# Optimization experiments

Measured on AMD Instinct MI355X. Metric: run time of the kernel, lower is better.

Reference implementation:

```python
import jax, jax.numpy as jnp
import numpy as np

N, M, D_M, D_S = 200000, 100000, 128, 128


def setup_inputs() -> dict:
    key = jax.random.key(0)
    ks = jax.random.split(key, 7)
    messages = jax.random.normal(ks[0], (M, D_M), dtype=jnp.float32)
    S = jax.random.normal(ks[1], (N, D_S), dtype=jnp.float32)
    # torch GRUCell default init: U(-1/sqrt(d_s), 1/sqrt(d_s))
    bound = 1.0 / np.sqrt(D_S)
    W_ih = jax.random.uniform(ks[2], (3 * D_S, D_M), minval=-bound, maxval=bound, dtype=jnp.float32)
    W_hh = jax.random.uniform(ks[3], (3 * D_S, D_S), minval=-bound, maxval=bound, dtype=jnp.float32)
    b_ih = jax.random.uniform(ks[4], (3 * D_S,), minval=-bound, maxval=bound, dtype=jnp.float32)
    b_hh = jax.random.uniform(ks[5], (3 * D_S,), minval=-bound, maxval=bound, dtype=jnp.float32)
    # dict keys are unique -> draw M unique node indices
    idx = jax.random.permutation(ks[6], N)[:M].astype(jnp.int64)
    return {"messages": messages, "S": S, "W_ih": W_ih, "W_hh": W_hh,
            "b_ih": b_ih, "b_hh": b_hh, "idx": idx}


def gru_cell(x, h, W_ih, W_hh, b_ih, b_hh):
    # torch.nn.GRUCell math, gate order (r, z, n)
    gi = x @ W_ih.T + b_ih          # [M, 3*d_s]
    gh = h @ W_hh.T + b_hh          # [M, 3*d_s]
    gi_r, gi_z, gi_n = jnp.split(gi, 3, axis=-1)
    gh_r, gh_z, gh_n = jnp.split(gh, 3, axis=-1)
    r = jax.nn.sigmoid(gi_r + gh_r)
    z = jax.nn.sigmoid(gi_z + gh_z)
    n = jnp.tanh(gi_n + r * gh_n)
    return (1.0 - z) * n + z * h


def reference(messages, S, W_ih, W_hh, b_ih, b_hh, idx):
    h = S[idx]                                     # gather [M, d_s]
    h_new = gru_cell(messages, h, W_ih, W_hh, b_ih, b_hh)
    # original initializes S_next = ones_like(S), then scatters updates
    return jnp.ones_like(S).at[idx].set(h_new)
```

## Files before the change

kernel.cpp:

```cpp
#include <hip/hip_runtime.h>
#include <hip/hip_bf16.h>
#include <stdint.h>

#define MM 100000
#define NN 200000
#define DD 128
#define BM 32
#define NT 3125
#define GRID 512

typedef __attribute__((ext_vector_type(8))) short short8;
typedef __attribute__((ext_vector_type(4))) float f32x4;
typedef __attribute__((ext_vector_type(2))) unsigned int u32x2;

__device__ __forceinline__ unsigned short f2bf(float f) {
    union { float f; uint32_t u; } v; v.f = f;
    return (unsigned short)((v.u + 0x7FFFu + ((v.u >> 16) & 1u)) >> 16);
}
__device__ __forceinline__ unsigned int pack_bf2(float lo, float hi) {
    union { float f; uint32_t u; } a, b; a.f = lo; b.f = hi;
    return ((a.u + 0x8000u) >> 16) | ((b.u + 0x8000u) & 0xFFFF0000u);
}
__device__ __forceinline__ float bf2f(unsigned short s) {
    union { uint32_t u; float f; } v; v.u = ((uint32_t)s) << 16;
    return v.f;
}
__device__ __forceinline__ float sigmoidf(float x) {
    return 1.0f / (1.0f + __expf(-x));
}
__device__ __forceinline__ float tanh_fast(float x) {
    return 2.0f / (1.0f + __expf(-2.0f * x)) - 1.0f;
}

__global__ void fill_ones(f32x4* __restrict__ out, int n4) {
    int i = blockIdx.x * blockDim.x + threadIdx.x;
    int stride = gridDim.x * blockDim.x;
    f32x4 ones = {1.f, 1.f, 1.f, 1.f};
    for (; i < n4; i += stride) out[i] = ones;
}

__global__ void clear_mark(uint32_t* __restrict__ mark32) {
    int i = blockIdx.x * blockDim.x + threadIdx.x;
    if (i < (NN + 3) / 4) mark32[i] = 0;
}

__global__ void mark_rows(const int* __restrict__ idx, uint8_t* __restrict__ mark) {
    int m = blockIdx.x * blockDim.x + threadIdx.x;
    if (m < MM) mark[idx[m]] = 1;
}

__global__ void conv_w(const float* __restrict__ wih, const float* __restrict__ whh,
                       unsigned short* __restrict__ dst) {
    int i = blockIdx.x * blockDim.x + threadIdx.x;
    if (i < 3 * DD * DD) {
        dst[i] = f2bf(wih[i]);
        dst[3 * DD * DD + i] = f2bf(whh[i]);
    }
}

template <bool WBF16>
__device__ __forceinline__ short8 load_wfrag(const void* W, int row, int kbase) {
    if constexpr (WBF16) {
        const unsigned short* p = (const unsigned short*)W;
        return *reinterpret_cast<const short8*>(p + (size_t)row * DD + kbase);
    } else {
        const float* p = (const float*)W + (size_t)row * DD + kbase;
        f32x4 a = *reinterpret_cast<const f32x4*>(p);
        f32x4 b = *reinterpret_cast<const f32x4*>(p + 4);
        short8 r;
        r[0] = (short)f2bf(a[0]); r[1] = (short)f2bf(a[1]);
        r[2] = (short)f2bf(a[2]); r[3] = (short)f2bf(a[3]);
        r[4] = (short)f2bf(b[0]); r[5] = (short)f2bf(b[1]);
        r[6] = (short)f2bf(b[2]); r[7] = (short)f2bf(b[3]);
        return r;
    }
}

template <bool WBF16>
__global__ __launch_bounds__(512, 4) void gru_kernel(
    const float* __restrict__ msgs, const float* __restrict__ S,
    const void* __restrict__ Wih, const void* __restrict__ Whh,
    const float* __restrict__ b_ih, const float* __restrict__ b_hh,
    const int* __restrict__ idx, float* __restrict__ out,
    const uint8_t* __restrict__ mark)
{
    __shared__ unsigned short Xl[2][BM][136];
    __shared__ unsigned short Hl[2][BM][136];
    __shared__ int Il[2][BM];

    const int tid = threadIdx.x;
    const int wave = tid >> 6;
    const int lane = tid & 63;
    const int l15 = lane & 15;
    const int lk  = lane >> 4;
    const int c   = wave * 16 + l15;

    const float br   = b_ih[c] + b_hh[c];
    const float bz   = b_ih[DD + c] + b_hh[DD + c];
    const float bn_i = b_ih[2 * DD + c];
    const float bn_h = b_hh[2 * DD + c];

    const int srow = tid >> 5;
    const int sch  = tid & 31;

    int t = blockIdx.x;

    int si_g[2], si_n[2];
    f32x4 px[2], ph[2];
    #pragma unroll
    for (int it = 0; it < 2; ++it) si_g[it] = idx[t * BM + srow + it * 16];
    #pragma unroll
    for (int it = 0; it < 2; ++it) {
        int m = t * BM + srow + it * 16;
        px[it] = *reinterpret_cast<const f32x4*>(msgs + (size_t)m * DD + sch * 4);
        ph[it] = *reinterpret_cast<const f32x4*>(S + (size_t)si_g[it] * DD + sch * 4);
    }
    if (t + GRID < NT) {
        #pragma unroll
        for (int it = 0; it < 2; ++it) si_n[it] = idx[(t + GRID) * BM + srow + it * 16];
    }

    int p = 0;
    for (; t < NT; t += GRID) {
        const bool hasn = (t + GRID) < NT;

        #pragma unroll
        for (int it = 0; it < 2; ++it) {
            u32x2 xw, hw;
            xw[0] = pack_bf2(px[it][0], px[it][1]);
            xw[1] = pack_bf2(px[it][2], px[it][3]);
            hw[0] = pack_bf2(ph[it][0], ph[it][1]);
            hw[1] = pack_bf2(ph[it][2], ph[it][3]);
            *reinterpret_cast<u32x2*>(&Xl[p][srow + it * 16][sch * 4]) = xw;
            *reinterpret_cast<u32x2*>(&Hl[p][srow + it * 16][sch * 4]) = hw;
            if (sch == 0) Il[p][srow + it * 16] = si_g[it];
        }
        __syncthreads();

        if (hasn) {
            #pragma unroll
            for (int it = 0; it < 2; ++it) {
                int m = (t + GRID) * BM + srow + it * 16;
                px[it] = *reinterpret_cast<const f32x4*>(msgs + (size_t)m * DD + sch * 4);
                ph[it] = *reinterpret_cast<const f32x4*>(S + (size_t)si_n[it] * DD + sch * 4);
                si_g[it] = si_n[it];
            }
            if (t + 2 * GRID < NT) {
                #pragma unroll
                for (int it = 0; it < 2; ++it)
                    si_n[it] = idx[(t + 2 * GRID) * BM + srow + it * 16];
            }
        }

        f32x4 accR[2], accZ[2], accNi[2], accNh[2];
        #pragma unroll
        for (int mt = 0; mt < 2; ++mt) {
            accR[mt] = (f32x4){0.f, 0.f, 0.f, 0.f};
            accZ[mt] = (f32x4){0.f, 0.f, 0.f, 0.f};
            accNi[mt] = (f32x4){0.f, 0.f, 0.f, 0.f};
            accNh[mt] = (f32x4){0.f, 0.f, 0.f, 0.f};
        }
        #pragma unroll
        for (int ks = 0; ks < 4; ++ks) {
            const int kb = ks * 32 + lk * 8;
            short8 ax[2], ah[2];
            #pragma unroll
            for (int mt = 0; mt < 2; ++mt) {
                ax[mt] = *reinterpret_cast<const short8*>(&Xl[p][mt * 16 + l15][kb]);
                ah[mt] = *reinterpret_cast<const short8*>(&Hl[p][mt * 16 + l15][kb]);
            }
            short8 bRi = load_wfrag<WBF16>(Wih, c, kb);
            short8 bRh = load_wfrag<WBF16>(Whh, c, kb);
            short8 bZi = load_wfrag<WBF16>(Wih, DD + c, kb);
            short8 bZh = load_wfrag<WBF16>(Whh, DD + c, kb);
            short8 bNi = load_wfrag<WBF16>(Wih, 2 * DD + c, kb);
            short8 bNh = load_wfrag<WBF16>(Whh, 2 * DD + c, kb);
            #pragma unroll
            for (int mt = 0; mt < 2; ++mt) {
                accR[mt]  = __builtin_amdgcn_mfma_f32_16x16x32_bf16(ax[mt], bRi, accR[mt], 0, 0, 0);
                accR[mt]  = __builtin_amdgcn_mfma_f32_16x16x32_bf16(ah[mt], bRh, accR[mt], 0, 0, 0);
                accZ[mt]  = __builtin_amdgcn_mfma_f32_16x16x32_bf16(ax[mt], bZi, accZ[mt], 0, 0, 0);
                accZ[mt]  = __builtin_amdgcn_mfma_f32_16x16x32_bf16(ah[mt], bZh, accZ[mt], 0, 0, 0);
                accNi[mt] = __builtin_amdgcn_mfma_f32_16x16x32_bf16(ax[mt], bNi, accNi[mt], 0, 0, 0);
                accNh[mt] = __builtin_amdgcn_mfma_f32_16x16x32_bf16(ah[mt], bNh, accNh[mt], 0, 0, 0);
            }
        }

        #pragma unroll
        for (int mt = 0; mt < 2; ++mt) {
            #pragma unroll
            for (int j = 0; j < 4; ++j) {
                int mloc = mt * 16 + lk * 4 + j;
                float r = sigmoidf(accR[mt][j] + br);
                float z = sigmoidf(accZ[mt][j] + bz);
                float n = tanh_fast(accNi[mt][j] + bn_i + r * (accNh[mt][j] + bn_h));
                float h = bf2f(Hl[p][mloc][c]);
                uint32_t off = (uint32_t)Il[p][mloc] * (uint32_t)DD + (uint32_t)c;
                out[off] = (1.f - z) * n + z * h;
            }
        }
        p ^= 1;
    }

    if (mark != nullptr) {
        f32x4 ones = {1.f, 1.f, 1.f, 1.f};
        f32x4* out4 = (f32x4*)out;
        int g = blockIdx.x * 512 + tid;
        for (int i = g; i < NN * 32; i += GRID * 512)
            if (!mark[i >> 5]) out4[i] = ones;
    }
}

extern "C" void kernel_launch(void* const* d_in, const int* in_sizes, int n_in,
                              void* d_out, int out_size, void* d_ws, size_t ws_size,
                              hipStream_t stream) {
    const float* msgs  = (const float*)d_in[0];
    const float* S     = (const float*)d_in[1];
    const float* W_ih  = (const float*)d_in[2];
    const float* W_hh  = (const float*)d_in[3];
    const float* b_ih  = (const float*)d_in[4];
    const float* b_hh  = (const float*)d_in[5];
    const int*   idx   = (const int*)d_in[6];
    float* out = (float*)d_out;

    const size_t wbytes = (size_t)2 * 3 * DD * DD * sizeof(unsigned short);
    const size_t need = wbytes + NN + 256;

    if (ws_size >= need) {
        unsigned short* wbf = (unsigned short*)d_ws;
        uint8_t* mark = (uint8_t*)d_ws + wbytes;
        clear_mark<<<(NN / 4 + 511) / 512, 512, 0, stream>>>((uint32_t*)mark);
        mark_rows<<<(MM + 511) / 512, 512, 0, stream>>>(idx, mark);
        conv_w<<<(3 * DD * DD + 255) / 256, 256, 0, stream>>>(W_ih, W_hh, wbf);
        gru_kernel<true><<<GRID, 512, 0, stream>>>(msgs, S, wbf, wbf + 3 * DD * DD,
                                                   b_ih, b_hh, idx, out, mark);
    } else {
        fill_ones<<<2048, 256, 0, stream>>>((f32x4*)out, NN * DD / 4);
        gru_kernel<false><<<GRID, 512, 0, stream>>>(msgs, S, W_ih, W_hh,
                                                    b_ih, b_hh, idx, out, nullptr);
    }
}
```

Before: 295.3 us.

## Replace persistent double-buffered GRU loop with one block per 32-row tile

Drops the persistent grid-stride loop, with its register prefetch and double-buffered LDS, and launches one block per 32-row tile (3125 blocks). Each block loads its tile, runs the MFMAs split into an input-side and a hidden-side phase so fewer weight fragments are live at once, then applies the gate epilogue. The aim is to lower register and LDS pressure and let the hardware scheduler overlap tiles across many resident blocks instead of relying on manual prefetch. The trade-off is that weight fragments are reloaded per block rather than per loop iteration, and the ones-fill tail now strides over a much larger grid.

After: 287.4 us. 1.03x faster.

```diff
diff --git a/kernel.cpp b/kernel.cpp
--- a/kernel.cpp
+++ b/kernel.cpp
@@ -6,8 +6,7 @@
 #define NN 200000
 #define DD 128
 #define BM 32
-#define NT 3125
-#define GRID 512
+#define NB 3125
 
 typedef __attribute__((ext_vector_type(8))) short short8;
 typedef __attribute__((ext_vector_type(4))) float f32x4;
@@ -84,108 +83,84 @@
     const int* __restrict__ idx, float* __restrict__ out,
     const uint8_t* __restrict__ mark)
 {
-    __shared__ unsigned short Xl[2][BM][136];
-    __shared__ unsigned short Hl[2][BM][136];
-    __shared__ int Il[2][BM];
+    __shared__ unsigned short Xl[BM][136];
+    __shared__ unsigned short Hl[BM][136];
+    __shared__ int Il[BM];
 
     const int tid = threadIdx.x;
-    const int wave = tid >> 6;
-    const int lane = tid & 63;
-    const int l15 = lane & 15;
-    const int lk  = lane >> 4;
-    const int c   = wave * 16 + l15;
-
-    const float br   = b_ih[c] + b_hh[c];
-    const float bz   = b_ih[DD + c] + b_hh[DD + c];
-    const float bn_i = b_ih[2 * DD + c];
-    const float bn_h = b_hh[2 * DD + c];
-
-    const int srow = tid >> 5;
-    const int sch  = tid & 31;
-
-    int t = blockIdx.x;
-
-    int si_g[2], si_n[2];
-    f32x4 px[2], ph[2];
-    #pragma unroll
-    for (int it = 0; it < 2; ++it) si_g[it] = idx[t * BM + srow + it * 16];
-    #pragma unroll
-    for (int it = 0; it < 2; ++it) {
-        int m = t * BM + srow + it * 16;
-        px[it] = *reinterpret_cast<const f32x4*>(msgs + (size_t)m * DD + sch * 4);
-        ph[it] = *reinterpret_cast<const f32x4*>(S + (size_t)si_g[it] * DD + sch * 4);
-    }
-    if (t + GRID < NT) {
-        #pragma unroll
-        for (int it = 0; it < 2; ++it) si_n[it] = idx[(t + GRID) * BM + srow + it * 16];
-    }
-
-    int p = 0;
-    for (; t < NT; t += GRID) {
-        const bool hasn = (t + GRID) < NT;
-
+    const int t   = blockIdx.x;
+
+    {
+        const int srow = tid >> 5;
+        const int sch  = tid & 31;
         #pragma unroll
         for (int it = 0; it < 2; ++it) {
+            int m = t * BM + srow + it * 16;
+            int si = idx[m];
+            f32x4 xv = *reinterpret_cast<const f32x4*>(msgs + (size_t)m * DD + sch * 4);
+            f32x4 hv = *reinterpret_cast<const f32x4*>(S + (size_t)si * DD + sch * 4);
             u32x2 xw, hw;
-            xw[0] = pack_bf2(px[it][0], px[it][1]);
-            xw[1] = pack_bf2(px[it][2], px[it][3]);
-            hw[0] = pack_bf2(ph[it][0], ph[it][1]);
-            hw[1] = pack_bf2(ph[it][2], ph[it][3]);
-            *reinterpret_cast<u32x2*>(&Xl[p][srow + it * 16][sch * 4]) = xw;
-            *reinterpret_cast<u32x2*>(&Hl[p][srow + it * 16][sch * 4]) = hw;
-            if (sch == 0) Il[p][srow + it * 16] = si_g[it];
-        }
-        __syncthreads();
-
-        if (hasn) {
-            #pragma unroll
-            for (int it = 0; it < 2; ++it) {
-                int m = (t + GRID) * BM + srow + it * 16;
-                px[it] = *reinterpret_cast<const f32x4*>(msgs + (size_t)m * DD + sch * 4);
-                ph[it] = *reinterpret_cast<const f32x4*>(S + (size_t)si_n[it] * DD + sch * 4);
-                si_g[it] = si_n[it];
-            }
-            if (t + 2 * GRID < NT) {
-                #pragma unroll
-                for (int it = 0; it < 2; ++it)
-                    si_n[it] = idx[(t + 2 * GRID) * BM + srow + it * 16];
-            }
-        }
-
-        f32x4 accR[2], accZ[2], accNi[2], accNh[2];
-        #pragma unroll
-        for (int mt = 0; mt < 2; ++mt) {
-            accR[mt] = (f32x4){0.f, 0.f, 0.f, 0.f};
-            accZ[mt] = (f32x4){0.f, 0.f, 0.f, 0.f};
-            accNi[mt] = (f32x4){0.f, 0.f, 0.f, 0.f};
-            accNh[mt] = (f32x4){0.f, 0.f, 0.f, 0.f};
-        }
-        #pragma unroll
-        for (int ks = 0; ks < 4; ++ks) {
-            const int kb = ks * 32 + lk * 8;
-            short8 ax[2], ah[2];
-            #pragma unroll
-            for (int mt = 0; mt < 2; ++mt) {
-                ax[mt] = *reinterpret_cast<const short8*>(&Xl[p][mt * 16 + l15][kb]);
-                ah[mt] = *reinterpret_cast<const short8*>(&Hl[p][mt * 16 + l15][kb]);
-            }
-            short8 bRi = load_wfrag<WBF16>(Wih, c, kb);
-            short8 bRh = load_wfrag<WBF16>(Whh, c, kb);
-            short8 bZi = load_wfrag<WBF16>(Wih, DD + c, kb);
-            short8 bZh = load_wfrag<WBF16>(Whh, DD + c, kb);
-            short8 bNi = load_wfrag<WBF16>(Wih, 2 * DD + c, kb);
-            short8 bNh = load_wfrag<WBF16>(Whh, 2 * DD + c, kb);
-            #pragma unroll
-            for (int mt = 0; mt < 2; ++mt) {
-                accR[mt]  = __builtin_amdgcn_mfma_f32_16x16x32_bf16(ax[mt], bRi, accR[mt], 0, 0, 0);
-                accR[mt]  = __builtin_amdgcn_mfma_f32_16x16x32_bf16(ah[mt], bRh, accR[mt], 0, 0, 0);
-                accZ[mt]  = __builtin_amdgcn_mfma_f32_16x16x32_bf16(ax[mt], bZi, accZ[mt], 0, 0, 0);
-                accZ[mt]  = __builtin_amdgcn_mfma_f32_16x16x32_bf16(ah[mt], bZh, accZ[mt], 0, 0, 0);
-                accNi[mt] = __builtin_amdgcn_mfma_f32_16x16x32_bf16(ax[mt], bNi, accNi[mt], 0, 0, 0);
-                accNh[mt] = __builtin_amdgcn_mfma_f32_16x16x32_bf16(ah[mt], bNh, accNh[mt], 0, 0, 0);
-            }
-        }
-
+            xw[0] = pack_bf2(xv[0], xv[1]);
+            xw[1] = pack_bf2(xv[2], xv[3]);
+            hw[0] = pack_bf2(hv[0], hv[1]);
+            hw[1] = pack_bf2(hv[2], hv[3]);
+            *reinterpret_cast<u32x2*>(&Xl[srow + it * 16][sch * 4]) = xw;
+            *reinterpret_cast<u32x2*>(&Hl[srow + it * 16][sch * 4]) = hw;
+            if (sch == 0) Il[srow + it * 16] = si;
+        }
+    }
+    __syncthreads();
+
+    const int lane = tid & 63;
+    const int l15  = lane & 15;
+    const int lk   = lane >> 4;
+    const int c    = (tid >> 6) * 16 + l15;
+
+    f32x4 accR[2], accZ[2], accNi[2], accNh[2];
+    #pragma unroll
+    for (int mt = 0; mt < 2; ++mt) {
+        accR[mt] = (f32x4){0.f, 0.f, 0.f, 0.f};
+        accZ[mt] = (f32x4){0.f, 0.f, 0.f, 0.f};
+        accNi[mt] = (f32x4){0.f, 0.f, 0.f, 0.f};
+        accNh[mt] = (f32x4){0.f, 0.f, 0.f, 0.f};
+    }
+
+    #pragma unroll
+    for (int ks = 0; ks < 4; ++ks) {
+        const int kb = ks * 32 + lk * 8;
+        {
+            short8 a0 = *reinterpret_cast<const short8*>(&Xl[l15][kb]);
+            short8 a1 = *reinterpret_cast<const short8*>(&Xl[16 + l15][kb]);
+            short8 b0 = load_wfrag<WBF16>(Wih, c, kb);
+            short8 b1 = load_wfrag<WBF16>(Wih, DD + c, kb);
+            short8 b2 = load_wfrag<WBF16>(Wih, 2 * DD + c, kb);
+            accR[0]  = __builtin_amdgcn_mfma_f32_16x16x32_bf16(a0, b0, accR[0], 0, 0, 0);
+            accR[1]  = __builtin_amdgcn_mfma_f32_16x16x32_bf16(a1, b0, accR[1], 0, 0, 0);
+            accZ[0]  = __builtin_amdgcn_mfma_f32_16x16x32_bf16(a0, b1, accZ[0], 0, 0, 0);
+            accZ[1]  = __builtin_amdgcn_mfma_f32_16x16x32_bf16(a1, b1, accZ[1], 0, 0, 0);
+            accNi[0] = __builtin_amdgcn_mfma_f32_16x16x32_bf16(a0, b2, accNi[0], 0, 0, 0);
+            accNi[1] = __builtin_amdgcn_mfma_f32_16x16x32_bf16(a1, b2, accNi[1], 0, 0, 0);
+        }
+        {
+            short8 a0 = *reinterpret_cast<const short8*>(&Hl[l15][kb]);
+            short8 a1 = *reinterpret_cast<const short8*>(&Hl[16 + l15][kb]);
+            short8 b0 = load_wfrag<WBF16>(Whh, c, kb);
+            short8 b1 = load_wfrag<WBF16>(Whh, DD + c, kb);
+            short8 b2 = load_wfrag<WBF16>(Whh, 2 * DD + c, kb);
+            accR[0]  = __builtin_amdgcn_mfma_f32_16x16x32_bf16(a0, b0, accR[0], 0, 0, 0);
+            accR[1]  = __builtin_amdgcn_mfma_f32_16x16x32_bf16(a1, b0, accR[1], 0, 0, 0);
+            accZ[0]  = __builtin_amdgcn_mfma_f32_16x16x32_bf16(a0, b1, accZ[0], 0, 0, 0);
+            accZ[1]  = __builtin_amdgcn_mfma_f32_16x16x32_bf16(a1, b1, accZ[1], 0, 0, 0);
+            accNh[0] = __builtin_amdgcn_mfma_f32_16x16x32_bf16(a0, b2, accNh[0], 0, 0, 0);
+            accNh[1] = __builtin_amdgcn_mfma_f32_16x16x32_bf16(a1, b2, accNh[1], 0, 0, 0);
+        }
+    }
+
+    {
+        const float br   = b_ih[c] + b_hh[c];
+        const float bz   = b_ih[DD + c] + b_hh[DD + c];
+        const float bn_i = b_ih[2 * DD + c];
+        const float bn_h = b_hh[2 * DD + c];
         #pragma unroll
         for (int mt = 0; mt < 2; ++mt) {
             #pragma unroll
@@ -194,19 +169,17 @@
                 float r = sigmoidf(accR[mt][j] + br);
                 float z = sigmoidf(accZ[mt][j] + bz);
                 float n = tanh_fast(accNi[mt][j] + bn_i + r * (accNh[mt][j] + bn_h));
-                float h = bf2f(Hl[p][mloc][c]);
-                uint32_t off = (uint32_t)Il[p][mloc] * (uint32_t)DD + (uint32_t)c;
+                float h = bf2f(Hl[mloc][c]);
+                uint32_t off = (uint32_t)Il[mloc] * (uint32_t)DD + (uint32_t)c;
                 out[off] = (1.f - z) * n + z * h;
             }
         }
-        p ^= 1;
     }
 
     if (mark != nullptr) {
         f32x4 ones = {1.f, 1.f, 1.f, 1.f};
         f32x4* out4 = (f32x4*)out;
-        int g = blockIdx.x * 512 + tid;
-        for (int i = g; i < NN * 32; i += GRID * 512)
+        for (int i = blockIdx.x * 512 + tid; i < NN * 32; i += NB * 512)
             if (!mark[i >> 5]) out4[i] = ones;
     }
 }
@@ -232,11 +205,11 @@
         clear_mark<<<(NN / 4 + 511) / 512, 512, 0, stream>>>((uint32_t*)mark);
         mark_rows<<<(MM + 511) / 512, 512, 0, stream>>>(idx, mark);
         conv_w<<<(3 * DD * DD + 255) / 256, 256, 0, stream>>>(W_ih, W_hh, wbf);
-        gru_kernel<true><<<GRID, 512, 0, stream>>>(msgs, S, wbf, wbf + 3 * DD * DD,
-                                                   b_ih, b_hh, idx, out, mark);
+        gru_kernel<true><<<NB, 512, 0, stream>>>(msgs, S, wbf, wbf + 3 * DD * DD,
+                                                 b_ih, b_hh, idx, out, mark);
     } else {
         fill_ones<<<2048, 256, 0, stream>>>((f32x4*)out, NN * DD / 4);
-        gru_kernel<false><<<GRID, 512, 0, stream>>>(msgs, S, W_ih, W_hh,
-                                                    b_ih, b_hh, idx, out, nullptr);
-    }
-}
+        gru_kernel<false><<<NB, 512, 0, stream>>>(msgs, S, W_ih, W_hh,
+                                                  b_ih, b_hh, idx, out, nullptr);
+    }
+}
```
